# Kernel optimization log

Hardware: AMD Instinct MI355X
Metric: run time of the kernel (lower is better)

The kernel has to match this reference:

```python
import jax, jax.numpy as jnp
import numpy as np

B, T_FRAMES, N, D, H, HT = 2, 16, 256, 768, 12, 12
INNER = 2 * D  # ConditionedTransitionBlock expansion_factor=2

def _ln(x, eps=1e-5):
    m = jnp.mean(x, axis=-1, keepdims=True)
    v = jnp.var(x, axis=-1, keepdims=True)
    return (x - m) * jax.lax.rsqrt(v + eps)

def _adaln(a, s, snorm_w, scale_w, scale_b, shift_w):
    an = _ln(a)            # LayerNorm(dim), no affine
    sn = _ln(s) * snorm_w  # LayerNorm(dim_cond), weight only
    return jax.nn.sigmoid(sn @ scale_w + scale_b) * an + sn @ shift_w

def _forward(a, s, bias, timestamps,
             ada_snorm_w, ada_scale_w, ada_scale_b, ada_shift_w,
             pb_q_w, pb_q_b, pb_k_w, pb_v_w, pb_g_w, pb_o_w,
             op_w, op_b,
             tr_snorm_w, tr_scale_w, tr_scale_b, tr_shift_w,
             tr_gate_w, tr_ab_w, tr_ba_w, tr_out_w, tr_out_b,
             tmp_ln_w, tmp_ln_b, tmp_q_w, tmp_q_b, tmp_k_w, tmp_v_w,
             tmp_decay, tmp_o_w,
             mask, multiplicity, T):
    BT, Nn, Dd = a.shape
    Bb = BT // T
    dh = Dd // H
    # --- AdaLN ---
    b = _adaln(a, s, ada_snorm_w, ada_scale_w, ada_scale_b, ada_shift_w)
    # --- pair-bias spatial attention (compute_pair_bias=False: z already (B,N,N,H)) ---
    q = (b @ pb_q_w + pb_q_b).reshape(BT, Nn, H, dh)
    k = (b @ pb_k_w).reshape(BT, Nn, H, dh)
    v = (b @ pb_v_w).reshape(BT, Nn, H, dh)
    z = jnp.transpose(bias, (0, 3, 1, 2))     # (B, H, N, N)
    z = jnp.repeat(z, multiplicity, axis=0)   # expand over T -> (B*T, H, N, N)
    scores = jnp.einsum('bqhd,bkhd->bhqk', q, k) * (dh ** -0.5) + z
    scores = jnp.where(mask[:, None, None, :], scores, -1e6)
    attn = jax.nn.softmax(scores, axis=-1)
    o = jnp.einsum('bhqk,bkhd->bqhd', attn, v).reshape(BT, Nn, Dd)
    g = jax.nn.sigmoid(b @ pb_g_w)
    attn_out = (g * o) @ pb_o_w
    # gated output projection (sigmoid, weights init 0 / bias -2) multiplied into residual
    a = a + jax.nn.sigmoid(s @ op_w + op_b) * attn_out
    # --- temporal attention with decay over T frames ---
    x = a.reshape(Bb, T, Nn, Dd).transpose(0, 2, 1, 3)   # (B, N, T, D)
    h = _ln(x) * tmp_ln_w + tmp_ln_b
    dht = Dd // HT
    qt = (h @ tmp_q_w + tmp_q_b).reshape(Bb, Nn, T, HT, dht)
    kt = (h @ tmp_k_w).reshape(Bb, Nn, T, HT, dht)
    vt = (h @ tmp_v_w).reshape(Bb, Nn, T, HT, dht)
    dt = jnp.abs(timestamps[:, :, None] - timestamps[:, None, :])           # (B, T, T)
    tb = -jax.nn.softplus(tmp_decay)[None, :, None, None] * dt[:, None]     # (B, HT, T, T)
    sct = jnp.einsum('bnqhd,bnkhd->bnhqk', qt, kt) * (dht ** -0.5) + tb[:, None]
    att = jax.nn.softmax(sct, axis=-1)
    ot = jnp.einsum('bnhqk,bnkhd->bnqhd', att, vt).reshape(Bb, Nn, T, Dd) @ tmp_o_w
    x = x + ot  # residual inside temporal attention
    a = x.transpose(0, 2, 1, 3).reshape(BT, Nn, Dd)
    # --- conditioned transition (SwiGLU gated by sigmoid(Linear(s))) ---
    b2 = _adaln(a, s, tr_snorm_w, tr_scale_w, tr_scale_b, tr_shift_w)
    hid = jax.nn.silu(b2 @ tr_gate_w) * (b2 @ tr_ab_w)
    a = a + jax.nn.sigmoid(s @ tr_out_w + tr_out_b) * (hid @ tr_ba_w)
    return a  # post_layer_norm=False -> Identity

def setup_inputs():
    key = jax.random.key(0)
    ks = iter(jax.random.split(key, 48))
    f = lambda shape, sc=1.0: jax.random.normal(next(ks), shape, jnp.float32) * sc
    return {
        'a': f((B * T_FRAMES, N, D)),
        's': f((B * T_FRAMES, N, D)),
        'bias': f((B, N, N, H)),
        'mask': jnp.ones((B * T_FRAMES, N), dtype=bool),
        'timestamps': jnp.sort(jax.random.uniform(next(ks), (B, T_FRAMES)) * 10.0, axis=-1),
        'multiplicity': T_FRAMES,
        'T': T_FRAMES,
        'ada_snorm_w': jnp.ones((D,)), 'ada_scale_w': f((D, D), 0.02),
        'ada_scale_b': jnp.zeros((D,)), 'ada_shift_w': f((D, D), 0.02),
        'pb_q_w': f((D, D), 0.02), 'pb_q_b': jnp.zeros((D,)),
        'pb_k_w': f((D, D), 0.02), 'pb_v_w': f((D, D), 0.02),
        'pb_g_w': f((D, D), 0.02), 'pb_o_w': f((D, D), 0.02),
        'op_w': f((D, D), 0.02), 'op_b': jnp.full((D,), -2.0),
        'tr_snorm_w': jnp.ones((D,)), 'tr_scale_w': f((D, D), 0.02),
        'tr_scale_b': jnp.zeros((D,)), 'tr_shift_w': f((D, D), 0.02),
        'tr_gate_w': f((D, INNER), 0.02), 'tr_ab_w': f((D, INNER), 0.02),
        'tr_ba_w': f((INNER, D), 0.02),
        'tr_out_w': f((D, D), 0.02), 'tr_out_b': jnp.full((D,), -2.0),
        'tmp_ln_w': jnp.ones((D,)), 'tmp_ln_b': jnp.zeros((D,)),
        'tmp_q_w': f((D, D), 0.02), 'tmp_q_b': jnp.zeros((D,)),
        'tmp_k_w': f((D, D), 0.02), 'tmp_v_w': f((D, D), 0.02),
        'tmp_decay': jnp.full((HT,), 0.5), 'tmp_o_w': f((D, D), 0.02),
    }

def reference(a, s, bias, mask, timestamps, multiplicity, T,
              ada_snorm_w, ada_scale_w, ada_scale_b, ada_shift_w,
              pb_q_w, pb_q_b, pb_k_w, pb_v_w, pb_g_w, pb_o_w,
              op_w, op_b,
              tr_snorm_w, tr_scale_w, tr_scale_b, tr_shift_w,
              tr_gate_w, tr_ab_w, tr_ba_w, tr_out_w, tr_out_b,
              tmp_ln_w, tmp_ln_b, tmp_q_w, tmp_q_b, tmp_k_w, tmp_v_w,
              tmp_decay, tmp_o_w):
    return _forward(a, s, bias, timestamps,
                    ada_snorm_w, ada_scale_w, ada_scale_b, ada_shift_w,
                    pb_q_w, pb_q_b, pb_k_w, pb_v_w, pb_g_w, pb_o_w,
                    op_w, op_b,
                    tr_snorm_w, tr_scale_w, tr_scale_b, tr_shift_w,
                    tr_gate_w, tr_ab_w, tr_ba_w, tr_out_w, tr_out_b,
                    tmp_ln_w, tmp_ln_b, tmp_q_w, tmp_q_b, tmp_k_w, tmp_v_w,
                    tmp_decay, tmp_o_w,
                    mask, multiplicity, T)
```

## Files before the change

### kernel.cpp

```cpp
#include <hip/hip_runtime.h>

typedef short s16x8 __attribute__((ext_vector_type(8)));
typedef short s16x4 __attribute__((ext_vector_type(4)));
typedef float f32x4 __attribute__((ext_vector_type(4)));
typedef __bf16 bf16x8 __attribute__((ext_vector_type(8)));

__device__ __forceinline__ float bf2f(short u) {
  union { unsigned int i; float f; } c;
  c.i = ((unsigned int)(unsigned short)u) << 16;
  return c.f;
}
__device__ __forceinline__ short f2bf(float f) {
  union { float f; unsigned int i; } c; c.f = f;
  unsigned int r = c.i + 0x7FFFu + ((c.i >> 16) & 1u);
  return (short)(r >> 16);
}
__device__ __forceinline__ float sigmoidf_(float x) { return 1.f / (1.f + __expf(-x)); }

template <typename T>
__device__ __forceinline__ auto mfma_sel(T a, T b, f32x4 c, int)
    -> decltype(__builtin_amdgcn_mfma_f32_16x16x32_bf16(a, b, c, 0, 0, 0)) {
  return __builtin_amdgcn_mfma_f32_16x16x32_bf16(a, b, c, 0, 0, 0);
}
template <typename T>
__device__ __forceinline__ f32x4 mfma_sel(T a, T b, f32x4 c, long) {
  return __builtin_amdgcn_mfma_f32_16x16x32_bf16(
      __builtin_bit_cast(bf16x8, a), __builtin_bit_cast(bf16x8, b), c, 0, 0, 0);
}
__device__ __forceinline__ f32x4 MFMA16(s16x8 a, s16x8 b, f32x4 c) {
  return mfma_sel(a, b, c, 0);
}

__device__ __forceinline__ long upk(int m, int c, int nu) {
  return ((long)(m >> 4) * nu + (c >> 3)) * 128 + ((m & 15) << 3) + (c & 7);
}

#define OFF_WADA1    0u
#define OFF_WQKVG    2359296u
#define OFF_WO       7077888u
#define OFF_WGATES   8257536u
#define OFF_WTMPQKV  10616832u
#define OFF_WTMPO    14155776u
#define OFF_WADA2    15335424u
#define OFF_WTRANS   17694720u
#define OFF_WBA      22413312u
#define OFF_BIAS     24772608u
#define OFF_ZT       24812544u
#define OFF_AN1      31104000u
#define OFF_SN1      43686912u
#define OFF_SN2      56269824u
#define OFF_SBF      68852736u
#define OFF_CADA     81435648u
#define OFF_QKVG     106601472u
#define OFF_GATES    156933120u
#define OFF_OGO      182098944u
#define OFF_A1       194681856u

__global__ __launch_bounds__(256) void prep_all(
    const float* p0, const float* p1, const float* p2, const float* p3,
    const float* p4, const float* p5, const float* p6, const float* p7,
    const float* p8, const float* p9, const float* p10, const float* p11,
    const float* p12, const float* p13, const float* p14, const float* p15,
    const float* p16, const float* p17, short* wsb,
    const float* __restrict__ zsrc, const float* __restrict__ ada_scale_b,
    const float* __restrict__ pb_q_b, const float* __restrict__ op_b,
    const float* __restrict__ tr_out_b, const float* __restrict__ tmp_q_b,
    const float* __restrict__ tr_scale_b,
    float* __restrict__ biasbuf, short* __restrict__ zt,
    const float* __restrict__ a_in, const float* __restrict__ s_in,
    const float* __restrict__ lnw1, const float* __restrict__ lnw2,
    short* __restrict__ an1, short* __restrict__ sn1, short* __restrict__ sn2,
    short* __restrict__ sbf) {
  const int z = blockIdx.z;
  const int tid = threadIdx.y * 32 + threadIdx.x;
  if (z < 18) {
    struct E { int K, N, dst; };
    const E tab[18] = {
        {768, 768, 0},        {768, 768, 589824},
        {768, 768, 1179648},  {768, 768, 1769472},
        {768, 768, 2359296},  {768, 768, 2949120},
        {768, 768, 3538944},
        {768, 768, 4128768},  {768, 768, 4718592},
        {768, 768, 7667712},  {768, 768, 8257536},
        {768, 1536, 8847360}, {768, 1536, 10027008},
        {1536, 768, 11206656},
        {768, 768, 5308416},  {768, 768, 5898240}, {768, 768, 6488064},
        {768, 768, 7077888}};
    int K = tab[z].K, N = tab[z].N;
    int n0 = blockIdx.x << 5, k0 = blockIdx.y << 5;
    if (n0 >= N || k0 >= K) return;
    const float* src;
    switch (z) {
      case 0: src = p0; break;  case 1: src = p1; break;
      case 2: src = p2; break;  case 3: src = p3; break;
      case 4: src = p4; break;  case 5: src = p5; break;
      case 6: src = p6; break;  case 7: src = p7; break;
      case 8: src = p8; break;  case 9: src = p9; break;
      case 10: src = p10; break; case 11: src = p11; break;
      case 12: src = p12; break; case 13: src = p13; break;
      case 14: src = p14; break; case 15: src = p15; break;
      case 16: src = p16; break; default: src = p17; break;
    }
    short* dst = wsb + tab[z].dst;
    const int ku = K >> 3;
    __shared__ float tile[32][33];
    int tx = threadIdx.x, ty = threadIdx.y;
#pragma unroll
    for (int j = 0; j < 4; j++)
      tile[ty + j * 8][tx] = src[(long)(k0 + ty + j * 8) * N + n0 + tx];
    __syncthreads();
#pragma unroll
    for (int j = 0; j < 4; j++) {
      int n = n0 + ty + j * 8, k = k0 + tx;
      dst[upk(n, k, ku)] = f2bf(tile[tx][ty + j * 8]);
    }
  } else if (z == 18) {
    const int bid = blockIdx.y * 48 + blockIdx.x;
    if (bid < 512) {
      const int b = bid >> 8, qq = bid & 255;
      const float* src = zsrc + (long)bid * 3072 + tid * 12;
      f32x4 v0 = *(const f32x4*)(src);
      f32x4 v1 = *(const f32x4*)(src + 4);
      f32x4 v2 = *(const f32x4*)(src + 8);
      float vals[12] = {v0[0], v0[1], v0[2], v0[3], v1[0], v1[1],
                        v1[2], v1[3], v2[0], v2[1], v2[2], v2[3]};
#pragma unroll
      for (int h = 0; h < 12; h++)
        zt[(((long)(b * 12 + h) * 256 + qq) << 8) + tid] = f2bf(vals[h]);
    } else if (bid < 551) {
      int j = (bid - 512) * 256 + tid;
      if (j < 9984) {
        float v;
        if (j < 1536) v = (j < 768) ? ada_scale_b[j] : 0.f;
        else if (j < 4608) { int jj = j - 1536; v = (jj < 768) ? pb_q_b[jj] : 0.f; }
        else if (j < 6144) { int jj = j - 4608; v = (jj < 768) ? op_b[jj] : tr_out_b[jj - 768]; }
        else if (j < 8448) { int jj = j - 6144; v = (jj < 768) ? tmp_q_b[jj] : 0.f; }
        else { int jj = j - 8448; v = (jj < 768) ? tr_scale_b[jj] : 0.f; }
        biasbuf[j] = v;
      }
    }
  } else {
    const int bid = blockIdx.y * 48 + blockIdx.x;
    if (bid >= 2048) return;
    const int wave = tid >> 6, lane = tid & 63;
    const int row = (bid << 2) + wave;
    const float* ar = a_in + (long)row * 768;
    const float* sr = s_in + (long)row * 768;
    f32x4 av[3], sv[3];
    float s0 = 0, s1 = 0, s2 = 0, s3 = 0;
#pragma unroll
    for (int k = 0; k < 3; k++) {
      int col = (lane << 2) + (k << 8);
      av[k] = *(const f32x4*)(ar + col);
      sv[k] = *(const f32x4*)(sr + col);
#pragma unroll
      for (int e = 0; e < 4; e++) {
        s0 += av[k][e]; s1 += av[k][e] * av[k][e];
        s2 += sv[k][e]; s3 += sv[k][e] * sv[k][e];
      }
    }
#pragma unroll
    for (int o = 32; o; o >>= 1) {
      s0 += __shfl_xor(s0, o, 64); s1 += __shfl_xor(s1, o, 64);
      s2 += __shfl_xor(s2, o, 64); s3 += __shfl_xor(s3, o, 64);
    }
    const float inv768 = 1.f / 768.f;
    float ma = s0 * inv768, va = s1 * inv768 - ma * ma;
    float ia = rsqrtf(va + 1e-5f);
    float ms = s2 * inv768, vs = s3 * inv768 - ms * ms;
    float is_ = rsqrtf(vs + 1e-5f);
#pragma unroll
    for (int k = 0; k < 3; k++) {
      int col = (lane << 2) + (k << 8);
      long o = upk(row, col, 96);
      s16x4 o1, o2, o3, o4;
#pragma unroll
      for (int e = 0; e < 4; e++) {
        o1[e] = f2bf((av[k][e] - ma) * ia);
        float sn = (sv[k][e] - ms) * is_;
        o2[e] = f2bf(sn * lnw1[col + e]);
        o3[e] = f2bf(sn * lnw2[col + e]);
        o4[e] = f2bf(sv[k][e]);
      }
      *(s16x4*)(an1 + o) = o1;
      *(s16x4*)(sn1 + o) = o2;
      *(s16x4*)(sn2 + o) = o3;
      *(s16x4*)(sbf + o) = o4;
    }
  }
}

__global__ __launch_bounds__(256) void ln_affine(
    const float* __restrict__ in, const float* __restrict__ w,
    const float* __restrict__ b, short* __restrict__ out) {
  const int wave = threadIdx.x >> 6, lane = threadIdx.x & 63;
  const int row = (blockIdx.x << 2) + wave;
  const float* xr = in + (long)row * 768;
  f32x4 xv[3];
  float s0 = 0, s1 = 0;
#pragma unroll
  for (int k = 0; k < 3; k++) {
    int col = (lane << 2) + (k << 8);
    xv[k] = *(const f32x4*)(xr + col);
#pragma unroll
    for (int e = 0; e < 4; e++) { s0 += xv[k][e]; s1 += xv[k][e] * xv[k][e]; }
  }
#pragma unroll
  for (int o = 32; o; o >>= 1) { s0 += __shfl_xor(s0, o, 64); s1 += __shfl_xor(s1, o, 64); }
  const float inv768 = 1.f / 768.f;
  float m = s0 * inv768, v = s1 * inv768 - m * m;
  float inv = rsqrtf(v + 1e-5f);
#pragma unroll
  for (int k = 0; k < 3; k++) {
    int col = (lane << 2) + (k << 8);
    s16x4 p;
#pragma unroll
    for (int e = 0; e < 4; e++) {
      float y = (xv[k][e] - m) * inv;
      if (w) y = y * w[col + e] + b[col + e];
      p[e] = f2bf(y);
    }
    *(s16x4*)(out + upk(row, col, 96)) = p;
  }
}

template <int EP>
__device__ __forceinline__ void dev_gemm_pk(
    const short* __restrict__ A, const short* __restrict__ W,
    const float* __restrict__ bias, void* __restrict__ Cout,
    const float* __restrict__ res, const short* __restrict__ gate,
    int K, int ldC, int gld) {
  const int tid = threadIdx.x;
  const int wave = tid >> 6, lane = tid & 63;
  const int m0 = blockIdx.y << 7, n0 = blockIdx.x << 7;
  const int wm = (wave & 1) << 6, wn = (wave >> 1) << 6;
  const int q = lane >> 4, r = lane & 15;
  const int ku = K >> 3;
  const short* ap[4];
  const short* bp[4];
#pragma unroll
  for (int mt = 0; mt < 4; mt++)
    ap[mt] = A + (long)(((m0 + wm) >> 4) + mt) * ku * 128 + (lane << 3);
#pragma unroll
  for (int nt = 0; nt < 4; nt++)
    bp[nt] = W + (long)(((n0 + wn) >> 4) + nt) * ku * 128 + (lane << 3);
  f32x4 acc[4][4];
#pragma unroll
  for (int i = 0; i < 4; i++)
#pragma unroll
    for (int j = 0; j < 4; j++) acc[i][j] = (f32x4){0.f, 0.f, 0.f, 0.f};

  for (int kt = 0; kt < K; kt += 64) {
#pragma unroll
    for (int ks = 0; ks < 2; ks++) {
      s16x8 av[4], bv[4];
#pragma unroll
      for (int mt = 0; mt < 4; mt++)
        av[mt] = *(const s16x8*)(ap[mt] + (ks << 9));
#pragma unroll
      for (int nt = 0; nt < 4; nt++)
        bv[nt] = *(const s16x8*)(bp[nt] + (ks << 9));
#pragma unroll
      for (int mt = 0; mt < 4; mt++)
#pragma unroll
        for (int nt = 0; nt < 4; nt++)
          acc[mt][nt] = MFMA16(bv[nt], av[mt], acc[mt][nt]);
    }
#pragma unroll
    for (int mt = 0; mt < 4; mt++) ap[mt] += 1024;
#pragma unroll
    for (int nt = 0; nt < 4; nt++) bp[nt] += 1024;
  }
#pragma unroll
  for (int mt = 0; mt < 4; mt++) {
    const int gm = m0 + wm + (mt << 4) + r;
#pragma unroll
    for (int nt = 0; nt < 4; nt++) {
      const int gnb = n0 + wn + (nt << 4) + (q << 2);
      f32x4 v = acc[mt][nt];
      if (bias) {
        f32x4 b4 = *(const f32x4*)(bias + gnb);
        v += b4;
      }
      long o = (long)gm * ldC + gnb;
      if (EP == 0) {
        s16x4 p;
#pragma unroll
        for (int e = 0; e < 4; e++) p[e] = f2bf(v[e]);
        *(s16x4*)((short*)Cout + o) = p;
      } else if (EP == 1) {
        s16x4 p;
#pragma unroll
        for (int e = 0; e < 4; e++) p[e] = f2bf(sigmoidf_(v[e]));
        *(s16x4*)((short*)Cout + o) = p;
      } else if (EP == 2) {
        f32x4 r4 = *(const f32x4*)(res + o);
        *(f32x4*)((float*)Cout + o) = r4 + v;
      } else {
        f32x4 r4 = *(const f32x4*)(res + o);
        s16x4 g4 = *(const s16x4*)(gate + (long)gm * gld + gnb);
        f32x4 out;
#pragma unroll
        for (int e = 0; e < 4; e++) out[e] = r4[e] + bf2f(g4[e]) * v[e];
        *(f32x4*)((float*)Cout + o) = out;
      }
    }
  }
}

template <int MODE>
__device__ __forceinline__ void dev_gemm_dual_pk(
    const short* __restrict__ A, const short* __restrict__ W1,
    const short* __restrict__ W2, const float* __restrict__ bias,
    const short* __restrict__ an, short* __restrict__ out, int nuO) {
  const int tid = threadIdx.x;
  const int wave = tid >> 6, lane = tid & 63;
  const int m0 = blockIdx.y << 7, n0 = blockIdx.x << 6;
  const int wm = (wave & 1) << 6, wn = (wave >> 1) << 5;
  const int q = lane >> 4, r = lane & 15;
  const short* ap[4];
  const short* b1p[2];
  const short* b2p[2];
#pragma unroll
  for (int mt = 0; mt < 4; mt++)
    ap[mt] = A + (long)(((m0 + wm) >> 4) + mt) * 96 * 128 + (lane << 3);
#pragma unroll
  for (int nt = 0; nt < 2; nt++) {
    long nb = (long)(((n0 + wn) >> 4) + nt) * 96 * 128 + (lane << 3);
    b1p[nt] = W1 + nb;
    b2p[nt] = W2 + nb;
  }
  f32x4 acc1[4][2], acc2[4][2];
#pragma unroll
  for (int i = 0; i < 4; i++)
#pragma unroll
    for (int j = 0; j < 2; j++) {
      acc1[i][j] = (f32x4){0.f, 0.f, 0.f, 0.f};
      acc2[i][j] = (f32x4){0.f, 0.f, 0.f, 0.f};
    }
  for (int kt = 0; kt < 768; kt += 64) {
#pragma unroll
    for (int ks = 0; ks < 2; ks++) {
      s16x8 av[4], b1[2], b2[2];
#pragma unroll
      for (int mt = 0; mt < 4; mt++)
        av[mt] = *(const s16x8*)(ap[mt] + (ks << 9));
#pragma unroll
      for (int nt = 0; nt < 2; nt++) {
        b1[nt] = *(const s16x8*)(b1p[nt] + (ks << 9));
        b2[nt] = *(const s16x8*)(b2p[nt] + (ks << 9));
      }
#pragma unroll
      for (int mt = 0; mt < 4; mt++)
#pragma unroll
        for (int nt = 0; nt < 2; nt++) {
          acc1[mt][nt] = MFMA16(b1[nt], av[mt], acc1[mt][nt]);
          acc2[mt][nt] = MFMA16(b2[nt], av[mt], acc2[mt][nt]);
        }
    }
#pragma unroll
    for (int mt = 0; mt < 4; mt++) ap[mt] += 1024;
#pragma unroll
    for (int nt = 0; nt < 2; nt++) { b1p[nt] += 1024; b2p[nt] += 1024; }
  }
#pragma unroll
  for (int mt = 0; mt < 4; mt++) {
    const int gm = m0 + wm + (mt << 4) + r;
#pragma unroll
    for (int nt = 0; nt < 2; nt++) {
      const int gnb = n0 + wn + (nt << 4) + (q << 2);
      s16x4 p;
      if (MODE == 0) {
        f32x4 b4 = *(const f32x4*)(bias + gnb);
        s16x4 an4 = *(const s16x4*)(an + upk(gm, gnb, 96));
#pragma unroll
        for (int e = 0; e < 4; e++)
          p[e] = f2bf(sigmoidf_(acc1[mt][nt][e] + b4[e]) * bf2f(an4[e]) +
                      acc2[mt][nt][e]);
      } else {
#pragma unroll
        for (int e = 0; e < 4; e++) {
          float x = acc1[mt][nt][e];
          p[e] = f2bf(x * sigmoidf_(x) * acc2[mt][nt][e]);
        }
      }
      *(s16x4*)(out + upk(gm, gnb, nuO)) = p;
    }
  }
}

template <int EP>
__global__ __launch_bounds__(256) void gemm_pk(
    const short* __restrict__ A, const short* __restrict__ W,
    const float* __restrict__ bias, void* __restrict__ Cout,
    const float* __restrict__ res, const short* __restrict__ gate,
    int K, int ldC, int gld) {
  dev_gemm_pk<EP>(A, W, bias, Cout, res, gate, K, ldC, gld);
}

template <int MODE>
__global__ __launch_bounds__(256) void gemm_dual_pk(
    const short* __restrict__ A, const short* __restrict__ W1,
    const short* __restrict__ W2, const float* __restrict__ bias,
    const short* __restrict__ an, short* __restrict__ out, int nuO) {
  dev_gemm_dual_pk<MODE>(A, W1, W2, bias, an, out, nuO);
}

__global__ __launch_bounds__(256) void gemm_pair(
    const short* __restrict__ sbf, const short* __restrict__ wgates,
    const float* __restrict__ bias_g, short* __restrict__ gates,
    const short* __restrict__ sn1, const short* __restrict__ wada1,
    const float* __restrict__ bias_a, const short* __restrict__ an1,
    short* __restrict__ outb) {
  if (blockIdx.z == 0)
    dev_gemm_pk<1>(sbf, wgates, bias_g, (void*)gates, nullptr, nullptr,
                   768, 1536, 0);
  else
    dev_gemm_dual_pk<0>(sn1, wada1, wada1 + (long)768 * 768, bias_a, an1,
                        outb, 96);
}

__global__ __launch_bounds__(256) void attn_spatial(
    const short* __restrict__ qkvg, const short* __restrict__ zt, short* __restrict__ ogo) {
  __shared__ short sKP[256 * 64];
  __shared__ short sVt[64 * 256];
  const int tid = threadIdx.x;
  const int wave = tid >> 6, lane = tid & 63;
  const int qt = blockIdx.x, h = blockIdx.y, bt = blockIdx.z;
  const int b = bt >> 4;
  const int q0 = qt << 6;
  const long rowbase = (long)bt << 8;
  const int hoff = h << 6;

#pragma unroll
  for (int t = 0; t < 8; t++) {
    int c = (t << 8) + tid;
    int tok = c >> 3, kc = (c & 7) ^ (tok & 7);
    *(s16x8*)(sKP + (c << 3)) =
        *(const s16x8*)(qkvg + (rowbase + tok) * 3072 + 768 + hoff + (kc << 3));
  }
#pragma unroll
  for (int t = 0; t < 8; t++) {
    int u = (t << 8) + tid;
    int tok = u >> 3, dc = u & 7;
    s16x8 v8 = *(const s16x8*)(qkvg + (rowbase + tok) * 3072 + 1536 + hoff + (dc << 3));
#pragma unroll
    for (int e = 0; e < 8; e++) {
      int d = (dc << 3) + e;
      int ch = (tok >> 3) ^ (d & 7);
      sVt[((d << 5) + ch) * 8 + (tok & 7)] = v8[e];
    }
  }
  __syncthreads();

  const int q = lane >> 4, cc = lane & 15;
  f32x4 acc[16];
#pragma unroll
  for (int i = 0; i < 16; i++) acc[i] = (f32x4){0.f, 0.f, 0.f, 0.f};
  {
    const int arow = (wave << 4) + cc;
    const short* qrow = qkvg + (rowbase + q0 + arow) * 3072 + hoff;
#pragma unroll
    for (int ks = 0; ks < 2; ks++) {
      s16x8 av = *(const s16x8*)(qrow + (ks << 5) + (q << 3));
#pragma unroll
      for (int nt = 0; nt < 16; nt++) {
        int tok = (nt << 4) + cc;
        int chb = ((ks << 2) + q) ^ (tok & 7);
        s16x8 bv = *(const s16x8*)(sKP + ((tok << 3) + chb) * 8);
        acc[nt] = MFMA16(av, bv, acc[nt]);
      }
    }
  }
  const short* ztb = zt + (((long)(b * 12 + h) * 256 + q0 + (wave << 4)) << 8);
#pragma unroll
  for (int reg = 0; reg < 4; reg++) {
    int lr = (q << 2) + reg;
    float mx = -3.0e38f;
#pragma unroll
    for (int nt = 0; nt < 16; nt++) {
      float v = acc[nt][reg] * 0.125f + bf2f(ztb[lr * 256 + (nt << 4) + cc]);
      acc[nt][reg] = v;
      mx = fmaxf(mx, v);
    }
    mx = fmaxf(mx, __shfl_xor(mx, 1, 16));
    mx = fmaxf(mx, __shfl_xor(mx, 2, 16));
    mx = fmaxf(mx, __shfl_xor(mx, 4, 16));
    mx = fmaxf(mx, __shfl_xor(mx, 8, 16));
    float sum = 0.f;
#pragma unroll
    for (int nt = 0; nt < 16; nt++) {
      float e = __expf(acc[nt][reg] - mx);
      acc[nt][reg] = e; sum += e;
    }
    sum += __shfl_xor(sum, 1, 16);
    sum += __shfl_xor(sum, 2, 16);
    sum += __shfl_xor(sum, 4, 16);
    sum += __shfl_xor(sum, 8, 16);
    float inv = 1.f / sum;
#pragma unroll
    for (int nt = 0; nt < 16; nt++) acc[nt][reg] *= inv;
  }
  __syncthreads();
#pragma unroll
  for (int nt = 0; nt < 16; nt++) {
#pragma unroll
    for (int reg = 0; reg < 4; reg++) {
      int rP = (wave << 4) + (q << 2) + reg;
      int col = (nt << 4) + cc;
      int ch = (col >> 3) ^ (rP & 7);
      sKP[((rP << 5) + ch) * 8 + (col & 7)] = f2bf(acc[nt][reg]);
    }
  }
  __syncthreads();
  f32x4 oacc[4];
#pragma unroll
  for (int i = 0; i < 4; i++) oacc[i] = (f32x4){0.f, 0.f, 0.f, 0.f};
  const int prow = (wave << 4) + cc;
#pragma unroll
  for (int ksi = 0; ksi < 8; ksi++) {
    int cha = ((ksi << 2) + q) ^ (prow & 7);
    s16x8 pa = *(const s16x8*)(sKP + ((prow << 5) + cha) * 8);
#pragma unroll
    for (int dt = 0; dt < 4; dt++) {
      int d = (dt << 4) + cc;
      int chv = ((ksi << 2) + q) ^ (d & 7);
      s16x8 bv = *(const s16x8*)(sVt + ((d << 5) + chv) * 8);
      oacc[dt] = MFMA16(pa, bv, oacc[dt]);
    }
  }
#pragma unroll
  for (int dt = 0; dt < 4; dt++) {
#pragma unroll
    for (int reg = 0; reg < 4; reg++) {
      int rowt = q0 + (wave << 4) + (q << 2) + reg;
      int dcol = (dt << 4) + cc;
      long grow = rowbase + rowt;
      float gl = bf2f(qkvg[grow * 3072 + 2304 + hoff + dcol]);
      ogo[upk((int)grow, hoff + dcol, 96)] = f2bf(oacc[dt][reg] * sigmoidf_(gl));
    }
  }
}

__global__ __launch_bounds__(256) void attn_temporal(
    const short* __restrict__ qkvt, const float* __restrict__ ts,
    const float* __restrict__ decay_raw, short* __restrict__ out) {
  __shared__ short sKV[16 * 1544];
  const int bn = blockIdx.x;
  const int b = bn >> 8, n = bn & 255;
  const int tid = threadIdx.x;
#pragma unroll
  for (int t = 0; t < 12; t++) {
    int u = t * 256 + tid;
    int row = u / 192, cc = u % 192;
    *(s16x8*)(sKV + row * 1544 + cc * 8) =
        *(const s16x8*)(qkvt + ((long)(b * 16 + row) * 256 + n) * 2304 + 768 + cc * 8);
  }
  __syncthreads();
  const int h = tid >> 4, tq = tid & 15;
  if (h < 12) {
    const int hoff = h << 6;
    float dec = log1pf(__expf(decay_raw[h]));
    float tsq = ts[b * 16 + tq];
    s16x8 qv[8];
    const short* qrow = qkvt + ((long)(b * 16 + tq) * 256 + n) * 2304 + hoff;
#pragma unroll
    for (int dc = 0; dc < 8; dc++) qv[dc] = *(const s16x8*)(qrow + dc * 8);
    float sc[16];
#pragma unroll
    for (int tk = 0; tk < 16; tk++) {
      float dot = 0.f;
#pragma unroll
      for (int dc = 0; dc < 8; dc++) {
        s16x8 kv = *(const s16x8*)(sKV + tk * 1544 + hoff + dc * 8);
#pragma unroll
        for (int e = 0; e < 8; e++) dot += bf2f(qv[dc][e]) * bf2f(kv[e]);
      }
      sc[tk] = dot * 0.125f - dec * fabsf(tsq - ts[b * 16 + tk]);
    }
    float mx = sc[0];
#pragma unroll
    for (int tk = 1; tk < 16; tk++) mx = fmaxf(mx, sc[tk]);
    float sum = 0.f;
#pragma unroll
    for (int tk = 0; tk < 16; tk++) { sc[tk] = __expf(sc[tk] - mx); sum += sc[tk]; }
    float inv = 1.f / sum;
    float oa[64];
#pragma unroll
    for (int d = 0; d < 64; d++) oa[d] = 0.f;
#pragma unroll
    for (int tk = 0; tk < 16; tk++) {
      float wgt = sc[tk] * inv;
#pragma unroll
      for (int dc = 0; dc < 8; dc++) {
        s16x8 vv = *(const s16x8*)(sKV + tk * 1544 + 768 + hoff + dc * 8);
#pragma unroll
        for (int e = 0; e < 8; e++) oa[dc * 8 + e] += wgt * bf2f(vv[e]);
      }
    }
    int orow = (b * 16 + tq) * 256 + n;
#pragma unroll
    for (int dc = 0; dc < 8; dc++) {
      s16x8 o8;
#pragma unroll
      for (int e = 0; e < 8; e++) o8[e] = f2bf(oa[dc * 8 + e]);
      *(s16x8*)(out + upk(orow, hoff + (dc << 3), 96)) = o8;
    }
  }
}

extern "C" void kernel_launch(void* const* d_in, const int* in_sizes, int n_in,
                              void* d_out, int out_size, void* d_ws, size_t ws_size,
                              hipStream_t stream) {
  (void)in_sizes; (void)n_in; (void)out_size; (void)ws_size;
  const float* a_in      = (const float*)d_in[0];
  const float* s_in      = (const float*)d_in[1];
  const float* bias_in   = (const float*)d_in[2];
  const float* ts        = (const float*)d_in[4];
  const float* ada_snorm = (const float*)d_in[7];
  const float* ada_scale_w = (const float*)d_in[8];
  const float* ada_scale_b = (const float*)d_in[9];
  const float* ada_shift_w = (const float*)d_in[10];
  const float* pb_q_w = (const float*)d_in[11];
  const float* pb_q_b = (const float*)d_in[12];
  const float* pb_k_w = (const float*)d_in[13];
  const float* pb_v_w = (const float*)d_in[14];
  const float* pb_g_w = (const float*)d_in[15];
  const float* pb_o_w = (const float*)d_in[16];
  const float* op_w = (const float*)d_in[17];
  const float* op_b = (const float*)d_in[18];
  const float* tr_snorm = (const float*)d_in[19];
  const float* tr_scale_w = (const float*)d_in[20];
  const float* tr_scale_b = (const float*)d_in[21];
  const float* tr_shift_w = (const float*)d_in[22];
  const float* tr_gate_w = (const float*)d_in[23];
  const float* tr_ab_w = (const float*)d_in[24];
  const float* tr_ba_w = (const float*)d_in[25];
  const float* tr_out_w = (const float*)d_in[26];
  const float* tr_out_b = (const float*)d_in[27];
  const float* tmp_ln_w = (const float*)d_in[28];
  const float* tmp_ln_b = (const float*)d_in[29];
  const float* tmp_q_w = (const float*)d_in[30];
  const float* tmp_q_b = (const float*)d_in[31];
  const float* tmp_k_w = (const float*)d_in[32];
  const float* tmp_v_w = (const float*)d_in[33];
  const float* tmp_decay = (const float*)d_in[34];
  const float* tmp_o_w = (const float*)d_in[35];

  char* ws = (char*)d_ws;
  short* W16 = (short*)ws;
  short* WADA1 = (short*)(ws + OFF_WADA1);
  short* WQKVG = (short*)(ws + OFF_WQKVG);
  short* WO = (short*)(ws + OFF_WO);
  short* WGATES = (short*)(ws + OFF_WGATES);
  short* WTMPQKV = (short*)(ws + OFF_WTMPQKV);
  short* WTMPO = (short*)(ws + OFF_WTMPO);
  short* WADA2 = (short*)(ws + OFF_WADA2);
  short* WTRANS = (short*)(ws + OFF_WTRANS);
  short* WBA = (short*)(ws + OFF_WBA);
  float* BIASB = (float*)(ws + OFF_BIAS);
  short* ZT = (short*)(ws + OFF_ZT);
  short* AN1 = (short*)(ws + OFF_AN1);
  short* SN1 = (short*)(ws + OFF_SN1);
  short* SN2 = (short*)(ws + OFF_SN2);
  short* SBF = (short*)(ws + OFF_SBF);
  short* CADA = (short*)(ws + OFF_CADA);
  short* QKVG = (short*)(ws + OFF_QKVG);
  short* GATES = (short*)(ws + OFF_GATES);
  short* OGO = (short*)(ws + OFF_OGO);
  float* A1F = (float*)(ws + OFF_A1);
  float* OUTF = (float*)d_out;

  prep_all<<<dim3(48, 48, 20), dim3(32, 8, 1), 0, stream>>>(
      ada_scale_w, ada_shift_w, pb_q_w, pb_k_w, pb_v_w, pb_g_w, pb_o_w,
      op_w, tr_out_w, tr_scale_w, tr_shift_w, tr_gate_w, tr_ab_w, tr_ba_w,
      tmp_q_w, tmp_k_w, tmp_v_w, tmp_o_w, W16,
      bias_in, ada_scale_b, pb_q_b, op_b, tr_out_b, tmp_q_b, tr_scale_b,
      BIASB, ZT,
      a_in, s_in, ada_snorm, tr_snorm, AN1, SN1, SN2, SBF);
  gemm_pair<<<dim3(12, 64, 2), 256, 0, stream>>>(
      SBF, WGATES, BIASB + 4608, GATES, SN1, WADA1, BIASB + 0, AN1, SBF);
  gemm_pk<0><<<dim3(24, 64), 256, 0, stream>>>(SBF, WQKVG, BIASB + 1536, QKVG,
                                               nullptr, nullptr, 768, 3072, 0);
  attn_spatial<<<dim3(4, 12, 32), 256, 0, stream>>>(QKVG, ZT, OGO);
  gemm_pk<3><<<dim3(6, 64), 256, 0, stream>>>(OGO, WO, nullptr, A1F, a_in, GATES,
                                              768, 768, 1536);
  ln_affine<<<2048, 256, 0, stream>>>(A1F, tmp_ln_w, tmp_ln_b, AN1);
  gemm_pk<0><<<dim3(18, 64), 256, 0, stream>>>(AN1, WTMPQKV, BIASB + 6144, QKVG,
                                               nullptr, nullptr, 768, 2304, 0);
  attn_temporal<<<512, 256, 0, stream>>>(QKVG, ts, tmp_decay, OGO);
  gemm_pk<2><<<dim3(6, 64), 256, 0, stream>>>(OGO, WTMPO, nullptr, A1F, A1F,
                                              nullptr, 768, 768, 0);
  ln_affine<<<2048, 256, 0, stream>>>(A1F, nullptr, nullptr, SN1);
  gemm_dual_pk<0><<<dim3(12, 64), 256, 0, stream>>>(
      SN2, WADA2, WADA2 + (long)768 * 768, BIASB + 8448, SN1, SBF, 96);
  gemm_dual_pk<1><<<dim3(24, 64), 256, 0, stream>>>(
      SBF, WTRANS, WTRANS + (long)1536 * 768, nullptr, nullptr, CADA, 192);
  gemm_pk<3><<<dim3(6, 64), 256, 0, stream>>>(CADA, WBA, nullptr, OUTF, A1F,
                                              GATES + 768, 1536, 768, 1536);
}
```

Measured before the change: 697.7 us.

## Double-buffer GEMM register loads and swap grid axes for M-major block order

The packed GEMM and dual-GEMM inner loops now prefetch the next 64-wide K slice into a second register set while MFMAs run on the current one, so global-load latency can hide behind matrix math. Grid dimensions are also swapped so that blockIdx.x walks M tiles, meaning consecutive blocks share the same weight tile, which may change L2 reuse. The cost is higher register use from the doubled operand buffers, which could lower occupancy. The loop assumes an even number of K steps; K of 768 and 1536 both satisfy this.

After: 676.4 us. 1.03x faster.

```diff
diff --git a/kernel.cpp b/kernel.cpp
--- a/kernel.cpp
+++ b/kernel.cpp
@@ -224,6 +224,69 @@
   }
 }
 
+__device__ __forceinline__ void load_set_bt(
+    const short* (&ap)[4], const short* (&bp)[4],
+    s16x8 (&av)[2][4], s16x8 (&bv)[2][4]) {
+#pragma unroll
+  for (int ks = 0; ks < 2; ks++) {
+#pragma unroll
+    for (int mt = 0; mt < 4; mt++)
+      av[ks][mt] = *(const s16x8*)(ap[mt] + (ks << 9));
+#pragma unroll
+    for (int nt = 0; nt < 4; nt++)
+      bv[ks][nt] = *(const s16x8*)(bp[nt] + (ks << 9));
+  }
+#pragma unroll
+  for (int mt = 0; mt < 4; mt++) ap[mt] += 1024;
+#pragma unroll
+  for (int nt = 0; nt < 4; nt++) bp[nt] += 1024;
+}
+
+__device__ __forceinline__ void mfma_set_bt(
+    const s16x8 (&av)[2][4], const s16x8 (&bv)[2][4], f32x4 (&acc)[4][4]) {
+#pragma unroll
+  for (int ks = 0; ks < 2; ks++)
+#pragma unroll
+    for (int mt = 0; mt < 4; mt++)
+#pragma unroll
+      for (int nt = 0; nt < 4; nt++)
+        acc[mt][nt] = MFMA16(bv[ks][nt], av[ks][mt], acc[mt][nt]);
+}
+
+__device__ __forceinline__ void load_set_dual(
+    const short* (&ap)[4], const short* (&b1p)[2], const short* (&b2p)[2],
+    s16x8 (&av)[2][4], s16x8 (&b1)[2][2], s16x8 (&b2)[2][2]) {
+#pragma unroll
+  for (int ks = 0; ks < 2; ks++) {
+#pragma unroll
+    for (int mt = 0; mt < 4; mt++)
+      av[ks][mt] = *(const s16x8*)(ap[mt] + (ks << 9));
+#pragma unroll
+    for (int nt = 0; nt < 2; nt++) {
+      b1[ks][nt] = *(const s16x8*)(b1p[nt] + (ks << 9));
+      b2[ks][nt] = *(const s16x8*)(b2p[nt] + (ks << 9));
+    }
+  }
+#pragma unroll
+  for (int mt = 0; mt < 4; mt++) ap[mt] += 1024;
+#pragma unroll
+  for (int nt = 0; nt < 2; nt++) { b1p[nt] += 1024; b2p[nt] += 1024; }
+}
+
+__device__ __forceinline__ void mfma_set_dual(
+    const s16x8 (&av)[2][4], const s16x8 (&b1)[2][2], const s16x8 (&b2)[2][2],
+    f32x4 (&acc1)[4][2], f32x4 (&acc2)[4][2]) {
+#pragma unroll
+  for (int ks = 0; ks < 2; ks++)
+#pragma unroll
+    for (int mt = 0; mt < 4; mt++)
+#pragma unroll
+      for (int nt = 0; nt < 2; nt++) {
+        acc1[mt][nt] = MFMA16(b1[ks][nt], av[ks][mt], acc1[mt][nt]);
+        acc2[mt][nt] = MFMA16(b2[ks][nt], av[ks][mt], acc2[mt][nt]);
+      }
+}
+
 template <int EP>
 __device__ __forceinline__ void dev_gemm_pk(
     const short* __restrict__ A, const short* __restrict__ W,
@@ -232,7 +295,7 @@
     int K, int ldC, int gld) {
   const int tid = threadIdx.x;
   const int wave = tid >> 6, lane = tid & 63;
-  const int m0 = blockIdx.y << 7, n0 = blockIdx.x << 7;
+  const int m0 = blockIdx.x << 7, n0 = blockIdx.y << 7;
   const int wm = (wave & 1) << 6, wn = (wave >> 1) << 6;
   const int q = lane >> 4, r = lane & 15;
   const int ku = K >> 3;
@@ -250,26 +313,14 @@
 #pragma unroll
     for (int j = 0; j < 4; j++) acc[i][j] = (f32x4){0.f, 0.f, 0.f, 0.f};
 
-  for (int kt = 0; kt < K; kt += 64) {
-#pragma unroll
-    for (int ks = 0; ks < 2; ks++) {
-      s16x8 av[4], bv[4];
-#pragma unroll
-      for (int mt = 0; mt < 4; mt++)
-        av[mt] = *(const s16x8*)(ap[mt] + (ks << 9));
-#pragma unroll
-      for (int nt = 0; nt < 4; nt++)
-        bv[nt] = *(const s16x8*)(bp[nt] + (ks << 9));
-#pragma unroll
-      for (int mt = 0; mt < 4; mt++)
-#pragma unroll
-        for (int nt = 0; nt < 4; nt++)
-          acc[mt][nt] = MFMA16(bv[nt], av[mt], acc[mt][nt]);
-    }
-#pragma unroll
-    for (int mt = 0; mt < 4; mt++) ap[mt] += 1024;
-#pragma unroll
-    for (int nt = 0; nt < 4; nt++) bp[nt] += 1024;
+  s16x8 av0[2][4], bv0[2][4], av1[2][4], bv1[2][4];
+  const int nk = K >> 6;
+  load_set_bt(ap, bp, av0, bv0);
+  for (int ki = 0; ki < nk; ki += 2) {
+    load_set_bt(ap, bp, av1, bv1);
+    mfma_set_bt(av0, bv0, acc);
+    if (ki + 2 < nk) load_set_bt(ap, bp, av0, bv0);
+    mfma_set_bt(av1, bv1, acc);
   }
 #pragma unroll
   for (int mt = 0; mt < 4; mt++) {
@@ -315,7 +366,7 @@
     const short* __restrict__ an, short* __restrict__ out, int nuO) {
   const int tid = threadIdx.x;
   const int wave = tid >> 6, lane = tid & 63;
-  const int m0 = blockIdx.y << 7, n0 = blockIdx.x << 6;
+  const int m0 = blockIdx.x << 7, n0 = blockIdx.y << 6;
   const int wm = (wave & 1) << 6, wn = (wave >> 1) << 5;
   const int q = lane >> 4, r = lane & 15;
   const short* ap[4];
@@ -338,30 +389,13 @@
       acc1[i][j] = (f32x4){0.f, 0.f, 0.f, 0.f};
       acc2[i][j] = (f32x4){0.f, 0.f, 0.f, 0.f};
     }
-  for (int kt = 0; kt < 768; kt += 64) {
-#pragma unroll
-    for (int ks = 0; ks < 2; ks++) {
-      s16x8 av[4], b1[2], b2[2];
-#pragma unroll
-      for (int mt = 0; mt < 4; mt++)
-        av[mt] = *(const s16x8*)(ap[mt] + (ks << 9));
-#pragma unroll
-      for (int nt = 0; nt < 2; nt++) {
-        b1[nt] = *(const s16x8*)(b1p[nt] + (ks << 9));
-        b2[nt] = *(const s16x8*)(b2p[nt] + (ks << 9));
-      }
-#pragma unroll
-      for (int mt = 0; mt < 4; mt++)
-#pragma unroll
-        for (int nt = 0; nt < 2; nt++) {
-          acc1[mt][nt] = MFMA16(b1[nt], av[mt], acc1[mt][nt]);
-          acc2[mt][nt] = MFMA16(b2[nt], av[mt], acc2[mt][nt]);
-        }
-    }
-#pragma unroll
-    for (int mt = 0; mt < 4; mt++) ap[mt] += 1024;
-#pragma unroll
-    for (int nt = 0; nt < 2; nt++) { b1p[nt] += 1024; b2p[nt] += 1024; }
+  s16x8 a0[2][4], x0[2][2], y0[2][2], a1[2][4], x1[2][2], y1[2][2];
+  load_set_dual(ap, b1p, b2p, a0, x0, y0);
+  for (int ki = 0; ki < 12; ki += 2) {
+    load_set_dual(ap, b1p, b2p, a1, x1, y1);
+    mfma_set_dual(a0, x0, y0, acc1, acc2);
+    if (ki + 2 < 12) load_set_dual(ap, b1p, b2p, a0, x0, y0);
+    mfma_set_dual(a1, x1, y1, acc1, acc2);
   }
 #pragma unroll
   for (int mt = 0; mt < 4; mt++) {
@@ -678,24 +712,24 @@
       bias_in, ada_scale_b, pb_q_b, op_b, tr_out_b, tmp_q_b, tr_scale_b,
       BIASB, ZT,
       a_in, s_in, ada_snorm, tr_snorm, AN1, SN1, SN2, SBF);
-  gemm_pair<<<dim3(12, 64, 2), 256, 0, stream>>>(
+  gemm_pair<<<dim3(64, 12, 2), 256, 0, stream>>>(
       SBF, WGATES, BIASB + 4608, GATES, SN1, WADA1, BIASB + 0, AN1, SBF);
-  gemm_pk<0><<<dim3(24, 64), 256, 0, stream>>>(SBF, WQKVG, BIASB + 1536, QKVG,
+  gemm_pk<0><<<dim3(64, 24), 256, 0, stream>>>(SBF, WQKVG, BIASB + 1536, QKVG,
                                                nullptr, nullptr, 768, 3072, 0);
   attn_spatial<<<dim3(4, 12, 32), 256, 0, stream>>>(QKVG, ZT, OGO);
-  gemm_pk<3><<<dim3(6, 64), 256, 0, stream>>>(OGO, WO, nullptr, A1F, a_in, GATES,
+  gemm_pk<3><<<dim3(64, 6), 256, 0, stream>>>(OGO, WO, nullptr, A1F, a_in, GATES,
                                               768, 768, 1536);
   ln_affine<<<2048, 256, 0, stream>>>(A1F, tmp_ln_w, tmp_ln_b, AN1);
-  gemm_pk<0><<<dim3(18, 64), 256, 0, stream>>>(AN1, WTMPQKV, BIASB + 6144, QKVG,
+  gemm_pk<0><<<dim3(64, 18), 256, 0, stream>>>(AN1, WTMPQKV, BIASB + 6144, QKVG,
                                                nullptr, nullptr, 768, 2304, 0);
   attn_temporal<<<512, 256, 0, stream>>>(QKVG, ts, tmp_decay, OGO);
-  gemm_pk<2><<<dim3(6, 64), 256, 0, stream>>>(OGO, WTMPO, nullptr, A1F, A1F,
+  gemm_pk<2><<<dim3(64, 6), 256, 0, stream>>>(OGO, WTMPO, nullptr, A1F, A1F,
                                               nullptr, 768, 768, 0);
   ln_affine<<<2048, 256, 0, stream>>>(A1F, nullptr, nullptr, SN1);
-  gemm_dual_pk<0><<<dim3(12, 64), 256, 0, stream>>>(
+  gemm_dual_pk<0><<<dim3(64, 12), 256, 0, stream>>>(
       SN2, WADA2, WADA2 + (long)768 * 768, BIASB + 8448, SN1, SBF, 96);
-  gemm_dual_pk<1><<<dim3(24, 64), 256, 0, stream>>>(
+  gemm_dual_pk<1><<<dim3(64, 24), 256, 0, stream>>>(
       SBF, WTRANS, WTRANS + (long)1536 * 768, nullptr, nullptr, CADA, 192);
-  gemm_pk<3><<<dim3(6, 64), 256, 0, stream>>>(CADA, WBA, nullptr, OUTF, A1F,
+  gemm_pk<3><<<dim3(64, 6), 256, 0, stream>>>(CADA, WBA, nullptr, OUTF, A1F,
                                               GATES + 768, 1536, 768, 1536);
 }
```
